# Kernel optimization log

Measured on AMD Instinct MI355X. Metric: run time of the kernel, lower is better.

The kernel has to match this reference:

```python
import jax, jax.numpy as jnp
import numpy as np

B, S, D, H = 2, 2048, 1024, 16
DK = D // H


def setup_inputs() -> dict:
    key = jax.random.key(0)
    ks = jax.random.split(key, 11)
    s = 1.0 / np.sqrt(D)
    inp = {
        "q": jax.random.normal(ks[0], (B, S, D), jnp.float32),
        "k": jax.random.normal(ks[1], (B, S, D), jnp.float32),
        "v": jax.random.normal(ks[2], (B, S, D), jnp.float32),
        "mask": jnp.tril(jnp.ones((S, S), jnp.int32))[None, None],  # causal [1,1,S,S]
        "w_q": jax.random.normal(ks[3], (D, D), jnp.float32) * s,
        "b_q": jax.random.normal(ks[4], (D,), jnp.float32) * 0.01,
        "w_k": jax.random.normal(ks[5], (D, D), jnp.float32) * s,
        "b_k": jax.random.normal(ks[6], (D,), jnp.float32) * 0.01,
        "w_v": jax.random.normal(ks[7], (D, D), jnp.float32) * s,
        "b_v": jax.random.normal(ks[8], (D,), jnp.float32) * 0.01,
        "w_o": jax.random.normal(ks[9], (D, D), jnp.float32) * s,
        "b_o": jax.random.normal(ks[10], (D,), jnp.float32) * 0.01,
    }
    return inp


def reference(q, k, v, mask, w_q, b_q, w_k, b_k, w_v, b_v, w_o, b_o):
    # Linear projections (torch Linear: x @ W.T + b)
    query = q @ w_q.T + b_q  # [B,S,D]
    key_ = k @ w_k.T + b_k
    value = v @ w_v.T + b_v
    # split heads -> [B,H,S,DK]
    def split(x):
        return x.reshape(B, S, H, DK).transpose(0, 2, 1, 3)
    qh, kh, vh = split(query), split(key_), split(value)
    scores = jnp.einsum("bhqd,bhkd->bhqk", qh, kh) / jnp.sqrt(jnp.float32(DK))
    scores = jnp.where(mask == 0, jnp.float32(-1e9), scores)
    attn = jax.nn.softmax(scores, axis=-1)
    out = jnp.einsum("bhqk,bhkd->bhqd", attn, vh)  # [B,H,S,DK]
    out = out.transpose(0, 2, 1, 3).reshape(B, S, D)
    return out @ w_o.T + b_o
```

## Files before the change

kernel.cpp:

```cpp
#include <hip/hip_runtime.h>


typedef __attribute__((ext_vector_type(8))) short bf16x8;
typedef __attribute__((ext_vector_type(4))) float floatx4;
typedef __attribute__((ext_vector_type(4))) unsigned short u16x4;

#define S_LEN 2048
#define D_MODEL 1024
#define N_HEADS 16
#define D_HEAD 64
#define M_ROWS 4096
#define QSCALE 0.18033688011112042f

__device__ __forceinline__ unsigned short f32_to_bf16(float f) {
  unsigned int u = __builtin_bit_cast(unsigned int, f);
  u += 0x7FFFu + ((u >> 16) & 1u);
  return (unsigned short)(u >> 16);
}

__global__ __launch_bounds__(256) void cvt_w(
    const float* __restrict__ w0, const float* __restrict__ w1,
    const float* __restrict__ w2, const float* __restrict__ w3,
    unsigned short* __restrict__ dst) {
  const int z = blockIdx.y;
  const float* src = (z == 0) ? w0 : (z == 1) ? w1 : (z == 2) ? w2 : w3;
  unsigned short* d = dst + ((long)z << 20);
  const int n4 = 1 << 18;
  for (int i = blockIdx.x * 256 + threadIdx.x; i < n4; i += gridDim.x * 256) {
    float4 f = ((const float4*)src)[i];
    u16x4 o;
    o[0] = f32_to_bf16(f.x); o[1] = f32_to_bf16(f.y);
    o[2] = f32_to_bf16(f.z); o[3] = f32_to_bf16(f.w);
    ((u16x4*)d)[i] = o;
  }
}

__global__ __launch_bounds__(256) void cvt_x(
    const float* __restrict__ x0, const float* __restrict__ x1,
    const float* __restrict__ x2, unsigned short* __restrict__ dst) {
  const int z = blockIdx.y;
  const float* src = (z == 0) ? x0 : (z == 1) ? x1 : x2;
  unsigned short* d = dst + (long)z * M_ROWS * D_MODEL;
  const int n4 = (M_ROWS * D_MODEL) / 4;
  for (int i = blockIdx.x * 256 + threadIdx.x; i < n4; i += gridDim.x * 256) {
    float4 f = ((const float4*)src)[i];
    u16x4 o;
    o[0] = f32_to_bf16(f.x); o[1] = f32_to_bf16(f.y);
    o[2] = f32_to_bf16(f.z); o[3] = f32_to_bf16(f.w);
    ((u16x4*)d)[i] = o;
  }
}

#define GK 1024
#define GN 1024
#define LDP 40

template <bool XPRE>
__global__ __launch_bounds__(256, 3) void qkv_gemm(
    const float* __restrict__ Xq, const float* __restrict__ Xk, const float* __restrict__ Xv,
    const unsigned short* __restrict__ Xb,
    const unsigned short* __restrict__ Wb,
    const float* __restrict__ bq, const float* __restrict__ bk, const float* __restrict__ bv,
    unsigned short* __restrict__ Yq, unsigned short* __restrict__ Yk,
    unsigned short* __restrict__ Yvt) {
  __shared__ __align__(16) unsigned short As[128 * LDP];
  __shared__ __align__(16) unsigned short Bs[128 * LDP];

  const int z = blockIdx.z;
  const unsigned short* W = Wb + ((long)z << 20);
  const float* bias = (z == 0) ? bq : ((z == 1) ? bk : bv);

  const int r0 = blockIdx.x * 128;
  const int n0 = blockIdx.y * 128;
  const int tid = threadIdx.x;
  const int lane = tid & 63;
  const int wave = tid >> 6;
  const int quad = lane >> 4;
  const int ln = lane & 15;
  const int wm = (wave >> 1) * 64;
  const int wn = (wave & 1) * 64;

  floatx4 acc[4][4];
#pragma unroll
  for (int i = 0; i < 4; i++)
#pragma unroll
    for (int j = 0; j < 4; j++) acc[i][j] = (floatx4){0.f, 0.f, 0.f, 0.f};

  const int srow = tid >> 1;
  const int scol = (tid & 1) * 16;
  unsigned short* Asw = As + srow * LDP + scol;
  unsigned short* Bsw = Bs + srow * LDP + scol;
  const unsigned short* Bp = W + (long)(n0 + srow) * GK + scol;
  const float* ApF = nullptr;
  const unsigned short* ApH = nullptr;
  if constexpr (XPRE) {
    ApH = Xb + (long)z * M_ROWS * D_MODEL + (long)(r0 + srow) * GK + scol;
  } else {
    const float* X = (z == 0) ? Xq : ((z == 1) ? Xk : Xv);
    ApF = X + (long)(r0 + srow) * GK + scol;
  }

  for (int k0 = 0; k0 < GK; k0 += 32) {
    float4 b0 = *(const float4*)(Bp + k0);
    float4 b1 = *(const float4*)(Bp + k0 + 8);
    float4 a0, a1;
    if constexpr (XPRE) {
      a0 = *(const float4*)(ApH + k0);
      a1 = *(const float4*)(ApH + k0 + 8);
    } else {
      unsigned short ua[16] __attribute__((aligned(16)));
      float fa[16] __attribute__((aligned(16)));
      *(float4*)(fa + 0)  = *(const float4*)(ApF + k0 + 0);
      *(float4*)(fa + 4)  = *(const float4*)(ApF + k0 + 4);
      *(float4*)(fa + 8)  = *(const float4*)(ApF + k0 + 8);
      *(float4*)(fa + 12) = *(const float4*)(ApF + k0 + 12);
#pragma unroll
      for (int j = 0; j < 16; j++) ua[j] = f32_to_bf16(fa[j]);
      a0 = *(float4*)(ua);
      a1 = *(float4*)(ua + 8);
    }
    __syncthreads();
    *(float4*)(Asw) = a0;
    *(float4*)(Asw + 8) = a1;
    *(float4*)(Bsw) = b0;
    *(float4*)(Bsw + 8) = b1;
    __syncthreads();

    bf16x8 af[4], bfr[4];
#pragma unroll
    for (int mt = 0; mt < 4; mt++)
      af[mt] = *(const bf16x8*)(As + (wm + mt * 16 + ln) * LDP + quad * 8);
#pragma unroll
    for (int nt = 0; nt < 4; nt++)
      bfr[nt] = *(const bf16x8*)(Bs + (wn + nt * 16 + ln) * LDP + quad * 8);
#pragma unroll
    for (int mt = 0; mt < 4; mt++)
#pragma unroll
      for (int nt = 0; nt < 4; nt++)
        acc[mt][nt] = __builtin_amdgcn_mfma_f32_16x16x32_bf16(af[mt], bfr[nt], acc[mt][nt], 0, 0, 0);
  }

#pragma unroll
  for (int nt = 0; nt < 4; nt++) {
    const int n = n0 + wn + nt * 16 + ln;
    const float bv = bias[n];
#pragma unroll
    for (int mt = 0; mt < 4; mt++) {
      const int r = r0 + wm + mt * 16 + quad * 4;
      if (z == 2) {
        u16x4 pk;
#pragma unroll
        for (int reg = 0; reg < 4; reg++) pk[reg] = f32_to_bf16(acc[mt][nt][reg] + bv);
        *(u16x4*)(Yvt + (long)n * M_ROWS + r) = pk;
      } else if (z == 0) {
#pragma unroll
        for (int reg = 0; reg < 4; reg++)
          Yq[(long)(r + reg) * GN + n] = f32_to_bf16((acc[mt][nt][reg] + bv) * QSCALE);
      } else {
#pragma unroll
        for (int reg = 0; reg < 4; reg++)
          Yk[(long)(r + reg) * GN + n] = f32_to_bf16(acc[mt][nt][reg] + bv);
      }
    }
  }
}

__global__ __launch_bounds__(256, 3) void out_gemm(
    const unsigned short* __restrict__ X,
    const unsigned short* __restrict__ W,
    const float* __restrict__ bias,
    float* __restrict__ Y) {
  __shared__ __align__(16) unsigned short As[64 * LDP];
  __shared__ __align__(16) unsigned short Bs[128 * LDP];

  const int r0 = blockIdx.x * 64;
  const int n0 = blockIdx.y * 128;
  const int tid = threadIdx.x;
  const int lane = tid & 63;
  const int wave = tid >> 6;
  const int quad = lane >> 4;
  const int ln = lane & 15;
  const int wm = (wave >> 1) * 32;
  const int wn = (wave & 1) * 64;

  floatx4 acc[2][4];
#pragma unroll
  for (int i = 0; i < 2; i++)
#pragma unroll
    for (int j = 0; j < 4; j++) acc[i][j] = (floatx4){0.f, 0.f, 0.f, 0.f};

  const int arow = tid >> 2;
  const int acol = (tid & 3) * 8;
  const unsigned short* Ap = X + (long)(r0 + arow) * GK + acol;
  unsigned short* Asw = As + arow * LDP + acol;
  const int brow = tid >> 1;
  const int bcol = (tid & 1) * 16;
  const unsigned short* Bp = W + (long)(n0 + brow) * GK + bcol;
  unsigned short* Bsw = Bs + brow * LDP + bcol;

  for (int k0 = 0; k0 < GK; k0 += 32) {
    float4 a0 = *(const float4*)(Ap + k0);
    float4 b0 = *(const float4*)(Bp + k0);
    float4 b1 = *(const float4*)(Bp + k0 + 8);
    __syncthreads();
    *(float4*)(Asw) = a0;
    *(float4*)(Bsw) = b0;
    *(float4*)(Bsw + 8) = b1;
    __syncthreads();

    bf16x8 af[2], bfr[4];
#pragma unroll
    for (int mt = 0; mt < 2; mt++)
      af[mt] = *(const bf16x8*)(As + (wm + mt * 16 + ln) * LDP + quad * 8);
#pragma unroll
    for (int nt = 0; nt < 4; nt++)
      bfr[nt] = *(const bf16x8*)(Bs + (wn + nt * 16 + ln) * LDP + quad * 8);
#pragma unroll
    for (int mt = 0; mt < 2; mt++)
#pragma unroll
      for (int nt = 0; nt < 4; nt++)
        acc[mt][nt] = __builtin_amdgcn_mfma_f32_16x16x32_bf16(af[mt], bfr[nt], acc[mt][nt], 0, 0, 0);
  }

#pragma unroll
  for (int nt = 0; nt < 4; nt++) {
    const int n = n0 + wn + nt * 16 + ln;
    const float bv = bias[n];
#pragma unroll
    for (int mt = 0; mt < 2; mt++) {
      const int r = r0 + wm + mt * 16 + quad * 4;
#pragma unroll
      for (int reg = 0; reg < 4; reg++)
        Y[(long)(r + reg) * GN + n] = acc[mt][nt][reg] + bv;
    }
  }
}

#define PSTR 72

__global__ __launch_bounds__(64, 2) void attn_causal(
    const unsigned short* __restrict__ Q,
    const unsigned short* __restrict__ K,
    const unsigned short* __restrict__ Vt,
    unsigned short* __restrict__ O) {
  __shared__ __align__(16) unsigned short PbA[16 * PSTR];
  __shared__ __align__(16) unsigned short PbB[16 * PSTR];

  const int bh = blockIdx.x;
  const int pr = blockIdx.y;
  const int b = bh >> 4;
  const int h = bh & 15;

  const int lane = threadIdx.x;
  const int quad = lane >> 4;
  const int ln = lane & 15;

  const int s1 = pr, s2 = 127 - pr;
  const int q0A = s1 * 16, q0B = s2 * 16;
  const int nkt1 = (s1 >> 2) + 1;
  const int nkt2 = (s2 >> 2) + 1;

  const unsigned short* Qb = Q + (long)b * S_LEN * D_MODEL + h * D_HEAD;
  const unsigned short* Kb = K + (long)b * S_LEN * D_MODEL + h * D_HEAD;
  const unsigned short* Vb = Vt + (long)h * D_HEAD * M_ROWS + b * S_LEN;

  bf16x8 qfA[2], qfB[2];
  qfA[0] = *(const bf16x8*)(Qb + (long)(q0A + ln) * D_MODEL + quad * 8);
  qfA[1] = *(const bf16x8*)(Qb + (long)(q0A + ln) * D_MODEL + 32 + quad * 8);
  qfB[0] = *(const bf16x8*)(Qb + (long)(q0B + ln) * D_MODEL + quad * 8);
  qfB[1] = *(const bf16x8*)(Qb + (long)(q0B + ln) * D_MODEL + 32 + quad * 8);

  float mA = -1e30f, lA = 0.f, mB = -1e30f, lB = 0.f;
  floatx4 oA[4], oB[4];
#pragma unroll
  for (int nt = 0; nt < 4; nt++) {
    oA[nt] = (floatx4){0.f, 0.f, 0.f, 0.f};
    oB[nt] = (floatx4){0.f, 0.f, 0.f, 0.f};
  }

#pragma unroll 1
  for (int kt = 0; kt < nkt2; kt++) {
    const int kv0 = kt * 64;
    const bool aAct = (kt < nkt1);

    bf16x8 kf[4][2], vf[4][2];
#pragma unroll
    for (int ct = 0; ct < 4; ct++) {
      const unsigned short* kp = Kb + (long)(kv0 + ct * 16 + ln) * D_MODEL + quad * 8;
      kf[ct][0] = *(const bf16x8*)(kp);
      kf[ct][1] = *(const bf16x8*)(kp + 32);
    }
#pragma unroll
    for (int nt = 0; nt < 4; nt++) {
      const unsigned short* vp = Vb + (long)(nt * 16 + ln) * M_ROWS + kv0 + quad * 8;
      vf[nt][0] = *(const bf16x8*)(vp);
      vf[nt][1] = *(const bf16x8*)(vp + 32);
    }

    floatx4 sB[4], sA[4];
#pragma unroll
    for (int ct = 0; ct < 4; ct++) {
      sB[ct] = (floatx4){0.f, 0.f, 0.f, 0.f};
      sB[ct] = __builtin_amdgcn_mfma_f32_16x16x32_bf16(kf[ct][0], qfB[0], sB[ct], 0, 0, 0);
      sB[ct] = __builtin_amdgcn_mfma_f32_16x16x32_bf16(kf[ct][1], qfB[1], sB[ct], 0, 0, 0);
    }
    if (aAct) {
#pragma unroll
      for (int ct = 0; ct < 4; ct++) {
        sA[ct] = (floatx4){0.f, 0.f, 0.f, 0.f};
        sA[ct] = __builtin_amdgcn_mfma_f32_16x16x32_bf16(kf[ct][0], qfA[0], sA[ct], 0, 0, 0);
        sA[ct] = __builtin_amdgcn_mfma_f32_16x16x32_bf16(kf[ct][1], qfA[1], sA[ct], 0, 0, 0);
      }
    }

    {
      float tmax = -1e30f;
      if (kt == nkt2 - 1) {
        const int qg = q0B + ln;
#pragma unroll
        for (int ct = 0; ct < 4; ct++) {
          const int kvb = kv0 + ct * 16 + quad * 4;
#pragma unroll
          for (int reg = 0; reg < 4; reg++) {
            float sv = sB[ct][reg];
            if (kvb + reg > qg) sv = -1e30f;
            sB[ct][reg] = sv;
            tmax = fmaxf(tmax, sv);
          }
        }
      } else {
#pragma unroll
        for (int ct = 0; ct < 4; ct++)
#pragma unroll
          for (int reg = 0; reg < 4; reg++) tmax = fmaxf(tmax, sB[ct][reg]);
      }
      tmax = fmaxf(tmax, __shfl_xor(tmax, 16, 64));
      tmax = fmaxf(tmax, __shfl_xor(tmax, 32, 64));
      const float mnew = fmaxf(mB, tmax);
      const float alpha = exp2f(mB - mnew);
      mB = mnew;
      float rsum = 0.f;
#pragma unroll
      for (int ct = 0; ct < 4; ct++) {
        u16x4 pk;
#pragma unroll
        for (int reg = 0; reg < 4; reg++) {
          const float p = exp2f(sB[ct][reg] - mB);
          rsum += p;
          pk[reg] = f32_to_bf16(p);
        }
        *(u16x4*)(PbB + ln * PSTR + ct * 16 + quad * 4) = pk;
      }
      rsum += __shfl_xor(rsum, 16, 64);
      rsum += __shfl_xor(rsum, 32, 64);
      lB = lB * alpha + rsum;
#pragma unroll
      for (int nt = 0; nt < 4; nt++)
#pragma unroll
        for (int reg = 0; reg < 4; reg++) oB[nt][reg] *= alpha;
    }

    if (aAct) {
      float tmax = -1e30f;
      if (kt == nkt1 - 1) {
        const int qg = q0A + ln;
#pragma unroll
        for (int ct = 0; ct < 4; ct++) {
          const int kvb = kv0 + ct * 16 + quad * 4;
#pragma unroll
          for (int reg = 0; reg < 4; reg++) {
            float sv = sA[ct][reg];
            if (kvb + reg > qg) sv = -1e30f;
            sA[ct][reg] = sv;
            tmax = fmaxf(tmax, sv);
          }
        }
      } else {
#pragma unroll
        for (int ct = 0; ct < 4; ct++)
#pragma unroll
          for (int reg = 0; reg < 4; reg++) tmax = fmaxf(tmax, sA[ct][reg]);
      }
      tmax = fmaxf(tmax, __shfl_xor(tmax, 16, 64));
      tmax = fmaxf(tmax, __shfl_xor(tmax, 32, 64));
      const float mnew = fmaxf(mA, tmax);
      const float alpha = exp2f(mA - mnew);
      mA = mnew;
      float rsum = 0.f;
#pragma unroll
      for (int ct = 0; ct < 4; ct++) {
        u16x4 pk;
#pragma unroll
        for (int reg = 0; reg < 4; reg++) {
          const float p = exp2f(sA[ct][reg] - mA);
          rsum += p;
          pk[reg] = f32_to_bf16(p);
        }
        *(u16x4*)(PbA + ln * PSTR + ct * 16 + quad * 4) = pk;
      }
      rsum += __shfl_xor(rsum, 16, 64);
      rsum += __shfl_xor(rsum, 32, 64);
      lA = lA * alpha + rsum;
#pragma unroll
      for (int nt = 0; nt < 4; nt++)
#pragma unroll
        for (int reg = 0; reg < 4; reg++) oA[nt][reg] *= alpha;
    }

    __builtin_amdgcn_wave_barrier();

    {
      bf16x8 p0 = *(const bf16x8*)(PbB + ln * PSTR + quad * 8);
      bf16x8 p1 = *(const bf16x8*)(PbB + ln * PSTR + 32 + quad * 8);
#pragma unroll
      for (int nt = 0; nt < 4; nt++) {
        oB[nt] = __builtin_amdgcn_mfma_f32_16x16x32_bf16(vf[nt][0], p0, oB[nt], 0, 0, 0);
        oB[nt] = __builtin_amdgcn_mfma_f32_16x16x32_bf16(vf[nt][1], p1, oB[nt], 0, 0, 0);
      }
    }
    if (aAct) {
      bf16x8 p0 = *(const bf16x8*)(PbA + ln * PSTR + quad * 8);
      bf16x8 p1 = *(const bf16x8*)(PbA + ln * PSTR + 32 + quad * 8);
#pragma unroll
      for (int nt = 0; nt < 4; nt++) {
        oA[nt] = __builtin_amdgcn_mfma_f32_16x16x32_bf16(vf[nt][0], p0, oA[nt], 0, 0, 0);
        oA[nt] = __builtin_amdgcn_mfma_f32_16x16x32_bf16(vf[nt][1], p1, oA[nt], 0, 0, 0);
      }
    }
    __builtin_amdgcn_wave_barrier();
  }

  {
    const float inv = 1.0f / lA;
    unsigned short* op = O + (long)b * S_LEN * D_MODEL + (long)(q0A + ln) * D_MODEL + h * D_HEAD;
#pragma unroll
    for (int nt = 0; nt < 4; nt++) {
      u16x4 pk;
#pragma unroll
      for (int reg = 0; reg < 4; reg++) pk[reg] = f32_to_bf16(oA[nt][reg] * inv);
      *(u16x4*)(op + nt * 16 + quad * 4) = pk;
    }
  }
  {
    const float inv = 1.0f / lB;
    unsigned short* op = O + (long)b * S_LEN * D_MODEL + (long)(q0B + ln) * D_MODEL + h * D_HEAD;
#pragma unroll
    for (int nt = 0; nt < 4; nt++) {
      u16x4 pk;
#pragma unroll
      for (int reg = 0; reg < 4; reg++) pk[reg] = f32_to_bf16(oB[nt][reg] * inv);
      *(u16x4*)(op + nt * 16 + quad * 4) = pk;
    }
  }
}

extern "C" void kernel_launch(void* const* d_in, const int* in_sizes, int n_in,
                              void* d_out, int out_size, void* d_ws, size_t ws_size,
                              hipStream_t stream) {
  const float* q = (const float*)d_in[0];
  const float* k = (const float*)d_in[1];
  const float* v = (const float*)d_in[2];
  const float* w_q = (const float*)d_in[4];
  const float* b_q = (const float*)d_in[5];
  const float* w_k = (const float*)d_in[6];
  const float* b_k = (const float*)d_in[7];
  const float* w_v = (const float*)d_in[8];
  const float* b_v = (const float*)d_in[9];
  const float* w_o = (const float*)d_in[10];
  const float* b_o = (const float*)d_in[11];
  float* out = (float*)d_out;

  unsigned short* ws = (unsigned short*)d_ws;
  const long NE = (long)M_ROWS * D_MODEL;
  const bool xpre = (ws_size >= (size_t)7 * NE * sizeof(unsigned short));

  unsigned short *Qp, *Kp, *Vpt, *AO, *Wb, *Xb;
  if (xpre) {
    Qp = ws;
    Kp = ws + NE;
    Vpt = ws + 2 * NE;
    Wb = ws + 3 * NE;
    Xb = ws + 4 * NE;
    AO = ws + 4 * NE;
  } else {
    Qp = ws;
    Kp = ws + NE;
    Vpt = ws + 2 * NE;
    AO = ws + 3 * NE;
    Wb = ws + 4 * NE;
    Xb = nullptr;
  }

  cvt_w<<<dim3(256, 4), 256, 0, stream>>>(w_q, w_k, w_v, w_o, Wb);
  if (xpre) {
    cvt_x<<<dim3(512, 3), 256, 0, stream>>>(q, k, v, Xb);
    qkv_gemm<true><<<dim3(M_ROWS / 128, GN / 128, 3), 256, 0, stream>>>(
        q, k, v, Xb, Wb, b_q, b_k, b_v, Qp, Kp, Vpt);
  } else {
    qkv_gemm<false><<<dim3(M_ROWS / 128, GN / 128, 3), 256, 0, stream>>>(
        q, k, v, nullptr, Wb, b_q, b_k, b_v, Qp, Kp, Vpt);
  }
  attn_causal<<<dim3(2 * N_HEADS, 64), 64, 0, stream>>>(Qp, Kp, Vpt, AO);
  out_gemm<<<dim3(M_ROWS / 64, GN / 128), 256, 0, stream>>>(AO, Wb + 3 * (1 << 20), b_o, out);
}
```

Baseline: 284.6 us.

## Deepen GEMM K-tile to 64 and double-buffer K/V register loads in attention

```diff
diff --git a/kernel.cpp b/kernel.cpp
--- a/kernel.cpp
+++ b/kernel.cpp
@@ -53,7 +53,7 @@
 
 #define GK 1024
 #define GN 1024
-#define LDP 40
+#define LDP 72
 
 template <bool XPRE>
 __global__ __launch_bounds__(256, 3) void qkv_gemm(
@@ -87,7 +87,7 @@
     for (int j = 0; j < 4; j++) acc[i][j] = (floatx4){0.f, 0.f, 0.f, 0.f};
 
   const int srow = tid >> 1;
-  const int scol = (tid & 1) * 16;
+  const int scol = (tid & 1) * 32;
   unsigned short* Asw = As + srow * LDP + scol;
   unsigned short* Bsw = Bs + srow * LDP + scol;
   const unsigned short* Bp = W + (long)(n0 + srow) * GK + scol;
@@ -100,44 +100,50 @@
     ApF = X + (long)(r0 + srow) * GK + scol;
   }
 
-  for (int k0 = 0; k0 < GK; k0 += 32) {
+  for (int k0 = 0; k0 < GK; k0 += 64) {
     float4 b0 = *(const float4*)(Bp + k0);
     float4 b1 = *(const float4*)(Bp + k0 + 8);
-    float4 a0, a1;
+    float4 b2 = *(const float4*)(Bp + k0 + 16);
+    float4 b3 = *(const float4*)(Bp + k0 + 24);
+    float4 a0, a1, a2, a3;
     if constexpr (XPRE) {
       a0 = *(const float4*)(ApH + k0);
       a1 = *(const float4*)(ApH + k0 + 8);
+      a2 = *(const float4*)(ApH + k0 + 16);
+      a3 = *(const float4*)(ApH + k0 + 24);
     } else {
-      unsigned short ua[16] __attribute__((aligned(16)));
-      float fa[16] __attribute__((aligned(16)));
-      *(float4*)(fa + 0)  = *(const float4*)(ApF + k0 + 0);
-      *(float4*)(fa + 4)  = *(const float4*)(ApF + k0 + 4);
-      *(float4*)(fa + 8)  = *(const float4*)(ApF + k0 + 8);
-      *(float4*)(fa + 12) = *(const float4*)(ApF + k0 + 12);
-#pragma unroll
-      for (int j = 0; j < 16; j++) ua[j] = f32_to_bf16(fa[j]);
-      a0 = *(float4*)(ua);
-      a1 = *(float4*)(ua + 8);
+      unsigned short ua[32] __attribute__((aligned(16)));
+      float fa[32] __attribute__((aligned(16)));
+#pragma unroll
+      for (int c = 0; c < 8; c++)
+        *(float4*)(fa + c * 4) = *(const float4*)(ApF + k0 + c * 4);
+#pragma unroll
+      for (int j = 0; j < 32; j++) ua[j] = f32_to_bf16(fa[j]);
+      a0 = *(float4*)(ua); a1 = *(float4*)(ua + 8);
+      a2 = *(float4*)(ua + 16); a3 = *(float4*)(ua + 24);
     }
     __syncthreads();
-    *(float4*)(Asw) = a0;
-    *(float4*)(Asw + 8) = a1;
-    *(float4*)(Bsw) = b0;
-    *(float4*)(Bsw + 8) = b1;
+    *(float4*)(Asw) = a0;      *(float4*)(Asw + 8) = a1;
+    *(float4*)(Asw + 16) = a2; *(float4*)(Asw + 24) = a3;
+    *(float4*)(Bsw) = b0;      *(float4*)(Bsw + 8) = b1;
+    *(float4*)(Bsw + 16) = b2; *(float4*)(Bsw + 24) = b3;
     __syncthreads();
 
-    bf16x8 af[4], bfr[4];
-#pragma unroll
-    for (int mt = 0; mt < 4; mt++)
-      af[mt] = *(const bf16x8*)(As + (wm + mt * 16 + ln) * LDP + quad * 8);
-#pragma unroll
-    for (int nt = 0; nt < 4; nt++)
-      bfr[nt] = *(const bf16x8*)(Bs + (wn + nt * 16 + ln) * LDP + quad * 8);
-#pragma unroll
-    for (int mt = 0; mt < 4; mt++)
+#pragma unroll
+    for (int ks = 0; ks < 64; ks += 32) {
+      bf16x8 af[4], bfr[4];
+#pragma unroll
+      for (int mt = 0; mt < 4; mt++)
+        af[mt] = *(const bf16x8*)(As + (wm + mt * 16 + ln) * LDP + ks + quad * 8);
 #pragma unroll
       for (int nt = 0; nt < 4; nt++)
-        acc[mt][nt] = __builtin_amdgcn_mfma_f32_16x16x32_bf16(af[mt], bfr[nt], acc[mt][nt], 0, 0, 0);
+        bfr[nt] = *(const bf16x8*)(Bs + (wn + nt * 16 + ln) * LDP + ks + quad * 8);
+#pragma unroll
+      for (int mt = 0; mt < 4; mt++)
+#pragma unroll
+        for (int nt = 0; nt < 4; nt++)
+          acc[mt][nt] = __builtin_amdgcn_mfma_f32_16x16x32_bf16(af[mt], bfr[nt], acc[mt][nt], 0, 0, 0);
+    }
   }
 
 #pragma unroll
@@ -190,36 +196,42 @@
     for (int j = 0; j < 4; j++) acc[i][j] = (floatx4){0.f, 0.f, 0.f, 0.f};
 
   const int arow = tid >> 2;
-  const int acol = (tid & 3) * 8;
+  const int acol = (tid & 3) * 16;
   const unsigned short* Ap = X + (long)(r0 + arow) * GK + acol;
   unsigned short* Asw = As + arow * LDP + acol;
   const int brow = tid >> 1;
-  const int bcol = (tid & 1) * 16;
+  const int bcol = (tid & 1) * 32;
   const unsigned short* Bp = W + (long)(n0 + brow) * GK + bcol;
   unsigned short* Bsw = Bs + brow * LDP + bcol;
 
-  for (int k0 = 0; k0 < GK; k0 += 32) {
+  for (int k0 = 0; k0 < GK; k0 += 64) {
     float4 a0 = *(const float4*)(Ap + k0);
+    float4 a1 = *(const float4*)(Ap + k0 + 8);
     float4 b0 = *(const float4*)(Bp + k0);
     float4 b1 = *(const float4*)(Bp + k0 + 8);
+    float4 b2 = *(const float4*)(Bp + k0 + 16);
+    float4 b3 = *(const float4*)(Bp + k0 + 24);
     __syncthreads();
-    *(float4*)(Asw) = a0;
-    *(float4*)(Bsw) = b0;
-    *(float4*)(Bsw + 8) = b1;
+    *(float4*)(Asw) = a0;      *(float4*)(Asw + 8) = a1;
+    *(float4*)(Bsw) = b0;      *(float4*)(Bsw + 8) = b1;
+    *(float4*)(Bsw + 16) = b2; *(float4*)(Bsw + 24) = b3;
     __syncthreads();
 
-    bf16x8 af[2], bfr[4];
-#pragma unroll
-    for (int mt = 0; mt < 2; mt++)
-      af[mt] = *(const bf16x8*)(As + (wm + mt * 16 + ln) * LDP + quad * 8);
-#pragma unroll
-    for (int nt = 0; nt < 4; nt++)
-      bfr[nt] = *(const bf16x8*)(Bs + (wn + nt * 16 + ln) * LDP + quad * 8);
-#pragma unroll
-    for (int mt = 0; mt < 2; mt++)
+#pragma unroll
+    for (int ks = 0; ks < 64; ks += 32) {
+      bf16x8 af[2], bfr[4];
+#pragma unroll
+      for (int mt = 0; mt < 2; mt++)
+        af[mt] = *(const bf16x8*)(As + (wm + mt * 16 + ln) * LDP + ks + quad * 8);
 #pragma unroll
       for (int nt = 0; nt < 4; nt++)
-        acc[mt][nt] = __builtin_amdgcn_mfma_f32_16x16x32_bf16(af[mt], bfr[nt], acc[mt][nt], 0, 0, 0);
+        bfr[nt] = *(const bf16x8*)(Bs + (wn + nt * 16 + ln) * LDP + ks + quad * 8);
+#pragma unroll
+      for (int mt = 0; mt < 2; mt++)
+#pragma unroll
+        for (int nt = 0; nt < 4; nt++)
+          acc[mt][nt] = __builtin_amdgcn_mfma_f32_16x16x32_bf16(af[mt], bfr[nt], acc[mt][nt], 0, 0, 0);
+    }
   }
 
 #pragma unroll
@@ -278,24 +290,22 @@
     oB[nt] = (floatx4){0.f, 0.f, 0.f, 0.f};
   }
 
-#pragma unroll 1
-  for (int kt = 0; kt < nkt2; kt++) {
+  auto loadKV = [&](bf16x8 (&kf)[4][2], bf16x8 (&vf)[4][2], int kt) {
     const int kv0 = kt * 64;
-    const bool aAct = (kt < nkt1);
-
-    bf16x8 kf[4][2], vf[4][2];
 #pragma unroll
     for (int ct = 0; ct < 4; ct++) {
       const unsigned short* kp = Kb + (long)(kv0 + ct * 16 + ln) * D_MODEL + quad * 8;
       kf[ct][0] = *(const bf16x8*)(kp);
       kf[ct][1] = *(const bf16x8*)(kp + 32);
-    }
-#pragma unroll
-    for (int nt = 0; nt < 4; nt++) {
-      const unsigned short* vp = Vb + (long)(nt * 16 + ln) * M_ROWS + kv0 + quad * 8;
-      vf[nt][0] = *(const bf16x8*)(vp);
-      vf[nt][1] = *(const bf16x8*)(vp + 32);
-    }
+      const unsigned short* vp = Vb + (long)(ct * 16 + ln) * M_ROWS + kv0 + quad * 8;
+      vf[ct][0] = *(const bf16x8*)(vp);
+      vf[ct][1] = *(const bf16x8*)(vp + 32);
+    }
+  };
+
+  auto iter = [&](bf16x8 (&kf)[4][2], bf16x8 (&vf)[4][2], int kt) {
+    const int kv0 = kt * 64;
+    const bool aAct = (kt < nkt1);
 
     floatx4 sB[4], sA[4];
 #pragma unroll
@@ -428,6 +438,17 @@
       }
     }
     __builtin_amdgcn_wave_barrier();
+  };
+
+  bf16x8 kf0[4][2], vf0[4][2], kf1[4][2], vf1[4][2];
+  loadKV(kf0, vf0, 0);
+#pragma unroll 1
+  for (int kt = 0; kt < nkt2; kt += 2) {
+    if (kt + 1 < nkt2) loadKV(kf1, vf1, kt + 1);
+    iter(kf0, vf0, kt);
+    if (kt + 1 >= nkt2) break;
+    if (kt + 2 < nkt2) loadKV(kf0, vf0, kt + 2);
+    iter(kf1, vf1, kt + 1);
   }
 
   {
```

Result: no change. 283.1 us (-0.6%).
